# Kernel optimization log

Measured on AMD Instinct MI355X. Metric: run time of the kernel, lower is better.

Reference implementation:

```python
import jax, jax.numpy as jnp
import numpy as np

B, C, H, W = 128, 8, 144, 144
TW, OG = 5, 2          # token_window, off_grid
NCLS, DT = 6, 256      # num_cls, dim_token
ITC = C * H * TW       # in_token_channel = 5760
EPS = 1e-5


def setup_inputs() -> dict:
    key = jax.random.key(0)
    ks = jax.random.split(key, 40)
    n = jax.random.normal
    u = jax.random.uniform
    CW = C * W  # 1152
    inp = {
        'x': n(ks[0], (B, C, H, W), jnp.float32),
        # ext head: Conv1d(1152,256,1) -> BN(256) -> Conv1d(256,2,1)
        'ext_w1': n(ks[1], (256, CW)) * 0.02, 'ext_b1': jnp.zeros((256,)),
        'ext_g': jnp.ones((256,)), 'ext_bb': jnp.zeros((256,)),
        'ext_m': n(ks[2], (256,)) * 0.1, 'ext_v': u(ks[3], (256,), minval=0.5, maxval=1.5),
        'ext_w2': n(ks[4], (2, 256)) * 0.05, 'ext_b2': jnp.zeros((2,)),
        # cls head: Conv1d(1152,256,1) -> BN(256) -> Conv1d(256,144,1)
        'cls_w1': n(ks[5], (256, CW)) * 0.02, 'cls_b1': jnp.zeros((256,)),
        'cls_g': jnp.ones((256,)), 'cls_bb': jnp.zeros((256,)),
        'cls_m': n(ks[6], (256,)) * 0.1, 'cls_v': u(ks[7], (256,), minval=0.5, maxval=1.5),
        'cls_w2': n(ks[8], (W, 256)) * 0.05, 'cls_b2': jnp.zeros((W,)),
        # to_token Linear(5760,256) and class embeddings
        'tok_w': n(ks[9], (ITC, DT)) * 0.01, 'tok_b': jnp.zeros((DT,)),
        'emb': n(ks[10], (NCLS, DT)),
        # transformer (depth=1, heads=2, dim_head=32 -> inner=64)
        'ln1_g': jnp.ones((DT,)), 'ln1_b': jnp.zeros((DT,)),
        'qkv_w': n(ks[11], (DT, 3 * 64)) * 0.05,
        'out_w': n(ks[12], (64, DT)) * 0.05, 'out_b': jnp.zeros((DT,)),
        'ln2_g': jnp.ones((DT,)), 'ln2_b': jnp.zeros((DT,)),
        'ff_w1': n(ks[13], (DT, 512)) * 0.05, 'ff_b1': jnp.zeros((512,)),
        'ff_w2': n(ks[14], (512, DT)) * 0.05, 'ff_b2': jnp.zeros((DT,)),
        'lnf_g': jnp.ones((DT,)), 'lnf_b': jnp.zeros((DT,)),
        'fin_w': n(ks[15], (DT, ITC)) * 0.02, 'fin_b': jnp.zeros((ITC,)),
    }
    return inp


def _ln(z, g, b):
    mu = jnp.mean(z, -1, keepdims=True)
    var = jnp.var(z, -1, keepdims=True)
    return (z - mu) * jax.lax.rsqrt(var + EPS) * g + b


def reference(x, ext_w1, ext_b1, ext_g, ext_bb, ext_m, ext_v, ext_w2, ext_b2,
              cls_w1, cls_b1, cls_g, cls_bb, cls_m, cls_v, cls_w2, cls_b2,
              tok_w, tok_b, emb,
              ln1_g, ln1_b, qkv_w, out_w, out_b,
              ln2_g, ln2_b, ff_w1, ff_b1, ff_w2, ff_b2,
              lnf_g, lnf_b, fin_w, fin_b):

    def head(row, w1, b1, g, bet, m, v, w2, b2):
        # row: [B, C*W, H]; 1x1 conv = per-position GEMM, BN in eval mode
        h = jnp.einsum('oc,bch->boh', w1, row) + b1[:, None]
        h = (h - m[:, None]) * jax.lax.rsqrt(v[:, None] + EPS) * g[:, None] + bet[:, None]
        h = jnp.einsum('oc,bch->boh', w2, h) + b2[:, None]
        return jnp.transpose(h, (0, 2, 1))  # [B, H, out]

    def heads_on(xx):
        # 'b c h w -> b (c w) h' (c major, w minor)
        row = jnp.transpose(xx, (0, 1, 3, 2)).reshape(B, C * W, H)
        e = jax.nn.softmax(head(row, ext_w1, ext_b1, ext_g, ext_bb, ext_m, ext_v, ext_w2, ext_b2), axis=2)
        c = jax.nn.softmax(head(row, cls_w1, cls_b1, cls_g, cls_bb, cls_m, cls_v, cls_w2, cls_b2), axis=2)
        return e, c

    ext, cls = heads_on(x)
    xp = jnp.pad(x, ((0, 0), (0, 0), (0, 0), (OG, OG)))  # [B,C,H,W+4]

    argmax_col = jnp.argmax(cls, axis=2)                  # [B,H]
    idx = argmax_col[:, :, None] + jnp.arange(TW)         # window in padded coords

    def transformer(t):  # t: [B, N, DT]
        z = _ln(t, ln1_g, ln1_b)
        q, k, v = jnp.split(z @ qkv_w, 3, axis=-1)
        sp = lambda a: a.reshape(B, -1, 2, 32).transpose(0, 2, 1, 3)  # b h n d
        q, k, v = sp(q), sp(k), sp(v)
        att = jax.nn.softmax(jnp.einsum('bhnd,bhmd->bhnm', q, k) * (32 ** -0.5), axis=-1)
        o = jnp.einsum('bhnm,bhmd->bhnd', att, v).transpose(0, 2, 1, 3).reshape(B, -1, 64)
        t = o @ out_w + out_b + t
        z = _ln(t, ln2_g, ln2_b)
        t = jax.nn.gelu(z @ ff_w1 + ff_b1, approximate=False) @ ff_w2 + ff_b2 + t
        t = _ln(t, lnf_g, lnf_b)
        return (t @ fin_w + fin_b).reshape(B, -1, C, H, TW)  # [B,N,C,H,TW]

    def refine(xpad):
        g_idx = jnp.broadcast_to(idx[:, None], (B, C, H, TW))
        patches = jnp.take_along_axis(xpad, g_idx, axis=3)    # [B,C,H,TW]
        tok = patches.reshape(B, -1) @ tok_w + tok_b          # [B,DT]
        tokens = tok[:, None, :] + emb[None]                  # [B,NCLS,DT]
        refined = transformer(tokens)                         # [B,NCLS,C,H,TW]
        xpt = jnp.transpose(xpad, (0, 2, 3, 1))               # [B,H,Wp,C]
        bb = jnp.arange(B)[:, None, None]
        hh = jnp.arange(H)[None, :, None]
        for i in range(NCLS):
            xpt = xpt.at[bb, hh, idx].set(jnp.transpose(refined[:, i], (0, 2, 3, 1)))
        return jnp.transpose(xpt, (0, 3, 1, 2))

    xp = jax.lax.cond(jnp.mean(ext[:, :, 0]) > 0.3, refine, lambda a: a, xp)
    x2 = xp[:, :, :, OG:W + OG]
    ext2, cls2 = heads_on(x2)
    return ext, cls, ext2, cls2
```

## Files before the change

kernel.cpp:

```cpp
#include <hip/hip_runtime.h>
#include <math.h>

#define EPSF 1e-5f
#define GAPTH 2e-4f
#define NKS 2
#define KSL 576
#define RROWS 18432
#define LPAD 44


typedef __attribute__((ext_vector_type(8))) short short8v;
typedef __attribute__((ext_vector_type(4))) float f32x4;
typedef unsigned short ushort;
typedef unsigned int uint;

__device__ inline ushort f2bf(float f) {
    uint u = __float_as_uint(f);
    uint r = (u + 0x7FFFu + ((u >> 16) & 1u)) >> 16;
    return (ushort)r;
}
__device__ inline float bf2f(ushort h) { return __uint_as_float(((uint)h) << 16); }

__global__ __launch_bounds__(256) void wcomb_build(
    const float* __restrict__ w1e, const float* __restrict__ b1e, const float* __restrict__ ge,
    const float* __restrict__ bbe, const float* __restrict__ me, const float* __restrict__ ve,
    const float* __restrict__ w2e, const float* __restrict__ b2e,
    const float* __restrict__ w1c, const float* __restrict__ b1c, const float* __restrict__ gc,
    const float* __restrict__ bbc, const float* __restrict__ mc, const float* __restrict__ vc,
    const float* __restrict__ w2c, const float* __restrict__ b2c,
    float* __restrict__ Wc32, ushort* __restrict__ Wchi, ushort* __restrict__ Wclo,
    float* __restrict__ cconst, int* __restrict__ cand_count)
{
    __shared__ float coef[256];
    __shared__ float csum[4];
    const int j = blockIdx.x, kq = blockIdx.y, tid = threadIdx.x;
    const int lane = tid & 63, wid = tid >> 6;

    if (j == 0 && kq == 0 && tid == 0) *cand_count = 0;

    const float *w1 = nullptr, *w2row = nullptr, *b1 = nullptr, *g = nullptr,
                *bb = nullptr, *m = nullptr, *v = nullptr;
    float b2v = 0.f;
    int valid = 0;
    if (j < 144) {
        valid = 1; w1 = w1c; w2row = w2c + (size_t)j * 256;
        b1 = b1c; g = gc; bb = bbc; m = mc; v = vc; b2v = b2c[j];
    } else if (j < 146) {
        valid = 1; w1 = w1e; w2row = w2e + (size_t)(j - 144) * 256;
        b1 = b1e; g = ge; bb = bbe; m = me; v = ve; b2v = b2e[j - 144];
    }

    float cf = 0.f, cc = 0.f;
    if (valid) {
        float s = g[tid] * rsqrtf(v[tid] + EPSF);
        float w2v = w2row[tid];
        cf = w2v * s;
        cc = w2v * ((b1[tid] - m[tid]) * s + bb[tid]);
    }
    coef[tid] = cf;
    if (kq == 0) {
        float t = cc;
#pragma unroll
        for (int off = 32; off; off >>= 1) t += __shfl_xor(t, off);
        if (lane == 0) csum[wid] = t;
    }
    __syncthreads();
    if (kq == 0 && tid == 0)
        cconst[j] = valid ? ((csum[0] + csum[1]) + (csum[2] + csum[3]) + b2v) : 0.f;

    for (int k = kq * 288 + tid; k < (kq + 1) * 288; k += 256) {
        float acc = 0.f;
        if (valid) {
            float a0 = 0.f, a1 = 0.f, a2 = 0.f, a3 = 0.f;
            for (int o = 0; o < 256; o += 4) {
                a0 += coef[o]     * w1[(size_t)o * 1152 + k];
                a1 += coef[o + 1] * w1[(size_t)(o + 1) * 1152 + k];
                a2 += coef[o + 2] * w1[(size_t)(o + 2) * 1152 + k];
                a3 += coef[o + 3] * w1[(size_t)(o + 3) * 1152 + k];
            }
            acc = (a0 + a1) + (a2 + a3);
        }
        Wc32[(size_t)j * 1152 + k] = acc;
        ushort hi = f2bf(acc);
        Wchi[(size_t)j * 1152 + k] = hi;
        Wclo[(size_t)j * 1152 + k] = f2bf(acc - bf2f(hi));
    }
}

__global__ __launch_bounds__(256) void transpose3(
    const float* __restrict__ s0, float* __restrict__ d0,
    const float* __restrict__ s1, float* __restrict__ d1,
    const float* __restrict__ s2, float* __restrict__ d2)
{
    const float* src; float* dst; int R, Cc;
    if (blockIdx.z == 0)      { src = s0; dst = d0; R = 256; Cc = 1152; }
    else if (blockIdx.z == 1) { src = s1; dst = d1; R = 144; Cc = 256;
                                if (blockIdx.x >= 8 || blockIdx.y >= 5) return; }
    else                      { src = s2; dst = d2; R = 160; Cc = 1152;
                                if (blockIdx.y >= 5) return; }
    __shared__ float tile[32][33];
    const int rb = blockIdx.y * 32, cb = blockIdx.x * 32;
    const int tx = threadIdx.x & 31, ty = threadIdx.x >> 5;
#pragma unroll
    for (int i = ty; i < 32; i += 8) {
        int r = rb + i, c = cb + tx;
        tile[i][tx] = (r < R && c < Cc) ? src[(size_t)r * Cc + c] : 0.f;
    }
    __syncthreads();
#pragma unroll
    for (int i = ty; i < 32; i += 8) {
        int c = cb + i, r = rb + tx;
        if (c < Cc && r < R) dst[(size_t)c * R + r] = tile[tx][i];
    }
}

__global__ __launch_bounds__(256) void logits_gemm(
    const float* __restrict__ x, const ushort* __restrict__ Wchi, const ushort* __restrict__ Wclo,
    float* __restrict__ logits_part)
{
    __shared__ ushort Ahi[64][LPAD], Alo[64][LPAD], Bhi[160][LPAD], Blo[160][LPAD];
    const int tid = threadIdx.x;
    const int lane = tid & 63, wid = tid >> 6;
    const int wm = wid & 1, wn = wid >> 1;
    const int rb = blockIdx.x * 64;
    const int ks = blockIdx.y;
    const int kbase = ks * KSL;
    const int NIT = KSL / 32;

    const int rl = tid >> 2, kk = (tid & 3) << 3;
    const int arow = rb + rl;
    const int ab = arow / 144, ahh = arow - ab * 144;

    const int br0 = tid >> 2, bk0 = (tid & 3) << 3;
    const int br2 = 128 + (tid >> 2), bk2 = (tid & 3) << 3;

    float av[8];
    short8v vbh0, vbl0, vbh1, vbl1, vbh2, vbl2;

    auto LOAD = [&](int kb) {
        int k1 = kb + kk, c1 = k1 / 144, w1 = k1 - c1 * 144;
        const float4 t0 = *reinterpret_cast<const float4*>(
            x + (((size_t)(ab * 8 + c1) * 144 + ahh) * 144 + w1));
        const float4 t1 = *reinterpret_cast<const float4*>(
            x + (((size_t)(ab * 8 + c1) * 144 + ahh) * 144 + w1 + 4));
        av[0] = t0.x; av[1] = t0.y; av[2] = t0.z; av[3] = t0.w;
        av[4] = t1.x; av[5] = t1.y; av[6] = t1.z; av[7] = t1.w;
        size_t o0 = (size_t)br0 * 1152 + kb + bk0;
        vbh0 = *reinterpret_cast<const short8v*>(Wchi + o0);
        vbl0 = *reinterpret_cast<const short8v*>(Wclo + o0);
        size_t o1 = (size_t)(br0 + 64) * 1152 + kb + bk0;
        vbh1 = *reinterpret_cast<const short8v*>(Wchi + o1);
        vbl1 = *reinterpret_cast<const short8v*>(Wclo + o1);
        if (tid < 128) {
            size_t o2 = (size_t)br2 * 1152 + kb + bk2;
            vbh2 = *reinterpret_cast<const short8v*>(Wchi + o2);
            vbl2 = *reinterpret_cast<const short8v*>(Wclo + o2);
        }
    };

    auto STORE = [&]() {
        short8v hv, lv;
#pragma unroll
        for (int q = 0; q < 8; q++) {
            ushort h = f2bf(av[q]);
            hv[q] = (short)h;
            lv[q] = (short)f2bf(av[q] - bf2f(h));
        }
        *reinterpret_cast<short8v*>(&Ahi[rl][kk]) = hv;
        *reinterpret_cast<short8v*>(&Alo[rl][kk]) = lv;
        *reinterpret_cast<short8v*>(&Bhi[br0][bk0]) = vbh0;
        *reinterpret_cast<short8v*>(&Blo[br0][bk0]) = vbl0;
        *reinterpret_cast<short8v*>(&Bhi[br0 + 64][bk0]) = vbh1;
        *reinterpret_cast<short8v*>(&Blo[br0 + 64][bk0]) = vbl1;
        if (tid < 128) {
            *reinterpret_cast<short8v*>(&Bhi[br2][bk2]) = vbh2;
            *reinterpret_cast<short8v*>(&Blo[br2][bk2]) = vbl2;
        }
    };

    f32x4 acc[2][5];
#pragma unroll
    for (int mt = 0; mt < 2; mt++)
#pragma unroll
        for (int nt = 0; nt < 5; nt++) acc[mt][nt] = (f32x4){0.f, 0.f, 0.f, 0.f};

    const int fr = lane & 15, fg = (lane >> 4) << 3;

    LOAD(kbase);
    for (int t = 0; t < NIT; t++) {
        STORE();
        __syncthreads();
        if (t < NIT - 1) LOAD(kbase + (t + 1) * 32);
        short8v ah0 = *reinterpret_cast<const short8v*>(&Ahi[wm * 32 + fr][fg]);
        short8v al0 = *reinterpret_cast<const short8v*>(&Alo[wm * 32 + fr][fg]);
        short8v ah1 = *reinterpret_cast<const short8v*>(&Ahi[wm * 32 + 16 + fr][fg]);
        short8v al1 = *reinterpret_cast<const short8v*>(&Alo[wm * 32 + 16 + fr][fg]);
#pragma unroll
        for (int nt = 0; nt < 5; nt++) {
            short8v bh = *reinterpret_cast<const short8v*>(&Bhi[wn * 80 + nt * 16 + fr][fg]);
            short8v bl = *reinterpret_cast<const short8v*>(&Blo[wn * 80 + nt * 16 + fr][fg]);
            acc[0][nt] = __builtin_amdgcn_mfma_f32_16x16x32_bf16(ah0, bh, acc[0][nt], 0, 0, 0);
            acc[0][nt] = __builtin_amdgcn_mfma_f32_16x16x32_bf16(ah0, bl, acc[0][nt], 0, 0, 0);
            acc[0][nt] = __builtin_amdgcn_mfma_f32_16x16x32_bf16(al0, bh, acc[0][nt], 0, 0, 0);
            acc[1][nt] = __builtin_amdgcn_mfma_f32_16x16x32_bf16(ah1, bh, acc[1][nt], 0, 0, 0);
            acc[1][nt] = __builtin_amdgcn_mfma_f32_16x16x32_bf16(ah1, bl, acc[1][nt], 0, 0, 0);
            acc[1][nt] = __builtin_amdgcn_mfma_f32_16x16x32_bf16(al1, bh, acc[1][nt], 0, 0, 0);
        }
        __syncthreads();
    }

    float* base = logits_part + (size_t)ks * RROWS * 160;
#pragma unroll
    for (int mt = 0; mt < 2; mt++) {
#pragma unroll
        for (int nt = 0; nt < 5; nt++) {
            int gcol = wn * 80 + nt * 16 + fr;
            if (gcol < 146) {
                float* dst = base + (size_t)(rb + wm * 32 + mt * 16 + ((lane >> 4) << 2)) * 160 + gcol;
#pragma unroll
                for (int i = 0; i < 4; i++)
                    dst[(size_t)i * 160] = acc[mt][nt][i];
            }
        }
    }
}

template<int DELTA>
__global__ __launch_bounds__(256) void softmax_heads(
    const float* __restrict__ logits_part, const float* __restrict__ cconst,
    float* __restrict__ out_cls, float* __restrict__ out_ext,
    int* __restrict__ amax, float* __restrict__ partials,
    int* __restrict__ cand_count, int* __restrict__ cand_list,
    const float* __restrict__ x, const float* __restrict__ WcT,
    const float* __restrict__ refined5, const int* __restrict__ flag)
{
    __shared__ float ps[4];
    __shared__ float dL[4][148];
    __shared__ float dsh[4][40];
    __shared__ int   ksh[4][40];
    const int r4 = threadIdx.x >> 6, lane = threadIdx.x & 63;
    const int row = blockIdx.x * 4 + r4;

    if (DELTA) {
        const int fl = *flag;
        if (fl) {
            const int b = row / 144, hh = row - b * 144;
            const int a = amax[row];
            if (lane < 40) {
                int c = lane / 5, tw = lane - c * 5;
                int w = a - 2 + tw;
                float d = 0.f; int k = 0;
                if (w >= 0 && w < 144) {
                    k = c * 144 + w;
                    d = refined5[(size_t)b * 5760 + (c * 144 + hh) * 5 + tw]
                      - x[((size_t)(b * 8 + c) * 144 + hh) * 144 + w];
                }
                dsh[r4][lane] = d; ksh[r4][lane] = k;
            }
            __syncthreads();
#pragma unroll
            for (int rj = 0; rj < 3; rj++) {
                int j = lane + rj * 64;
                if (j < 146) {
                    float acc = 0.f;
#pragma unroll 8
                    for (int i = 0; i < 40; i++)
                        acc += WcT[(size_t)ksh[r4][i] * 160 + j] * dsh[r4][i];
                    dL[r4][j] = acc;
                }
            }
        } else {
#pragma unroll
            for (int rj = 0; rj < 3; rj++) {
                int j = lane + rj * 64;
                if (j < 146) dL[r4][j] = 0.f;
            }
        }
        __syncthreads();
    }

    const float* L0 = logits_part + (size_t)row * 160;
    const float* L1 = L0 + (size_t)RROWS * 160;
    float v0 = L0[lane] + L1[lane] + cconst[lane];
    float v1 = L0[lane + 64] + L1[lane + 64] + cconst[lane + 64];
    float v2 = (lane < 16) ? (L0[lane + 128] + L1[lane + 128] + cconst[lane + 128])
                           : -3.0e38f;
    if (DELTA) {
        v0 += dL[r4][lane];
        v1 += dL[r4][lane + 64];
        if (lane < 16) v2 += dL[r4][lane + 128];
    }
    float m = v0; int mi = lane;
    if (v1 > m) { m = v1; mi = lane + 64; }
    if (v2 > m) { m = v2; mi = lane + 128; }
    float m1 = v0, m2 = -3.0e38f;
    if (v1 > m1) { m2 = m1; m1 = v1; } else m2 = v1;
    if (v2 > m1) { m2 = m1; m1 = v2; } else m2 = fmaxf(m2, v2);
#pragma unroll
    for (int off = 32; off; off >>= 1) {
        float om = __shfl_xor(m, off);
        int   oi = __shfl_xor(mi, off);
        if (om > m || (om == m && oi < mi)) { m = om; mi = oi; }
        float om1 = __shfl_xor(m1, off);
        float om2 = __shfl_xor(m2, off);
        float nm1 = fmaxf(m1, om1);
        m2 = fmaxf(fminf(m1, om1), fmaxf(m2, om2));
        m1 = nm1;
    }
    float e0 = expf(v0 - m), e1 = expf(v1 - m);
    float e2 = (lane < 16) ? expf(v2 - m) : 0.f;
    float s = e0 + e1 + e2;
#pragma unroll
    for (int off = 32; off; off >>= 1) s += __shfl_xor(s, off);
    float inv = 1.f / s;
    float* O = out_cls + (size_t)row * 144;
    O[lane] = e0 * inv;
    O[lane + 64] = e1 * inv;
    if (lane < 16) O[lane + 128] = e2 * inv;

    float l0 = L0[144] + L1[144] + cconst[144];
    float l1 = L0[145] + L1[145] + cconst[145];
    if (DELTA) { l0 += dL[r4][144]; l1 += dL[r4][145]; }
    float mx = fmaxf(l0, l1);
    float ee0 = expf(l0 - mx), ee1 = expf(l1 - mx);
    float einv = 1.f / (ee0 + ee1);
    float p0 = ee0 * einv;
    if (lane == 0) {
        out_ext[(size_t)row * 2] = p0;
        out_ext[(size_t)row * 2 + 1] = ee1 * einv;
        if (amax != nullptr && !DELTA) {
            amax[row] = mi;
            if (m1 - m2 < GAPTH) {
                int slot = atomicAdd(cand_count, 1);
                cand_list[slot] = row;
            }
        }
    }
    if (partials != nullptr) {
        if (lane == 0) ps[r4] = p0;
        __syncthreads();
        if (threadIdx.x == 0) partials[blockIdx.x] = (ps[0] + ps[1]) + (ps[2] + ps[3]);
    }
}

__global__ __launch_bounds__(256) void reduce_flag(const float* __restrict__ partials, int n,
                                                   int* __restrict__ flag)
{
    __shared__ float sm[256];
    int tid = threadIdx.x;
    float s = 0.f;
    for (int i = tid; i < n; i += 256) s += partials[i];
    sm[tid] = s; __syncthreads();
    for (int off = 128; off; off >>= 1) {
        if (tid < off) sm[tid] += sm[tid + off];
        __syncthreads();
    }
    if (tid == 0) *flag = (sm[0] * (1.f / 18432.f) > 0.3f) ? 1 : 0;
}

__global__ __launch_bounds__(256) void fixup_list(
    const int* __restrict__ cand_count, const int* __restrict__ cand_list,
    const float* __restrict__ x,
    const float* __restrict__ w1cT, const float* __restrict__ b1c,
    const float* __restrict__ gc, const float* __restrict__ bbc,
    const float* __restrict__ mc, const float* __restrict__ vc,
    const float* __restrict__ w2cT, const float* __restrict__ b2c,
    int* __restrict__ amax)
{
    __shared__ float xrow[1152];
    __shared__ float hsh[256];
    __shared__ float Lsh[144];
    const int tid = threadIdx.x;
    const int n = *cand_count;

    for (int ci = blockIdx.x; ci < n; ci += gridDim.x) {
        const int row = cand_list[ci];
        const int b = row / 144, hh = row - b * 144;
        for (int e = tid; e < 1152; e += 256) {
            int c = e / 144, w = e - c * 144;
            xrow[e] = x[(((size_t)(b * 8 + c) * 144 + hh) * 144) + w];
        }
        __syncthreads();
        {
            float a0 = 0.f, a1 = 0.f, a2 = 0.f, a3 = 0.f;
#pragma unroll 4
            for (int k = 0; k < 1152; k += 4) {
                a0 += w1cT[(size_t)k * 256 + tid] * xrow[k];
                a1 += w1cT[(size_t)(k + 1) * 256 + tid] * xrow[k + 1];
                a2 += w1cT[(size_t)(k + 2) * 256 + tid] * xrow[k + 2];
                a3 += w1cT[(size_t)(k + 3) * 256 + tid] * xrow[k + 3];
            }
            float a = (a0 + a1) + (a2 + a3);
            float sc = gc[tid] * rsqrtf(vc[tid] + EPSF);
            hsh[tid] = (a + b1c[tid] - mc[tid]) * sc + bbc[tid];
        }
        __syncthreads();
        if (tid < 144) {
            float a0 = 0.f, a1 = 0.f, a2 = 0.f, a3 = 0.f;
#pragma unroll 4
            for (int k = 0; k < 256; k += 4) {
                a0 += w2cT[(size_t)k * 144 + tid] * hsh[k];
                a1 += w2cT[(size_t)(k + 1) * 144 + tid] * hsh[k + 1];
                a2 += w2cT[(size_t)(k + 2) * 144 + tid] * hsh[k + 2];
                a3 += w2cT[(size_t)(k + 3) * 144 + tid] * hsh[k + 3];
            }
            Lsh[tid] = (a0 + a1) + (a2 + a3) + b2c[tid];
        }
        __syncthreads();
        if (tid == 0) {
            int bi = 0; float bv = Lsh[0];
            for (int j = 1; j < 144; j++) if (Lsh[j] > bv) { bv = Lsh[j]; bi = j; }
            amax[row] = bi;
        }
        __syncthreads();
    }
}

__global__ __launch_bounds__(256) void tok_partial(const float* __restrict__ x,
    const int* __restrict__ amax, const float* __restrict__ tok_w, float* __restrict__ tpart)
{
    __shared__ float P[720];
    __shared__ int ash[144];
    int b = blockIdx.x, c = blockIdx.y, tid = threadIdx.x;
    if (tid < 144) ash[tid] = amax[b * 144 + tid];
    __syncthreads();
    for (int e = tid; e < 720; e += 256) {
        int hh = e / 5, tw = e - hh * 5;
        int w = ash[hh] + tw - 2;
        P[e] = (w >= 0 && w < 144) ? x[(((size_t)(b * 8 + c) * 144 + hh) * 144) + w] : 0.f;
    }
    __syncthreads();
    const float* wbase = tok_w + (size_t)c * 720 * 256;
    float a0 = 0.f, a1 = 0.f, a2 = 0.f, a3 = 0.f;
    for (int k = 0; k < 720; k += 4) {
        a0 += P[k]     * wbase[(size_t)k * 256 + tid];
        a1 += P[k + 1] * wbase[(size_t)(k + 1) * 256 + tid];
        a2 += P[k + 2] * wbase[(size_t)(k + 2) * 256 + tid];
        a3 += P[k + 3] * wbase[(size_t)(k + 3) * 256 + tid];
    }
    tpart[((size_t)b * 8 + c) * 256 + tid] = (a0 + a1) + (a2 + a3);
}

__global__ __launch_bounds__(256) void qkv_gemm(
    const float* __restrict__ tpart, const float* __restrict__ tok_b,
    const float* __restrict__ emb,
    const float* __restrict__ ln1_g, const float* __restrict__ ln1_b,
    const float* __restrict__ qkv_w,
    float* __restrict__ qkbuf, float* __restrict__ sbuf)
{
    __shared__ float zrow[256];
    __shared__ float r8[8];
    const int b = blockIdx.x, y = blockIdx.y, tid = threadIdx.x;
    const int i = (y < 6) ? y : 5;
    const int lane = tid & 63, wv = tid >> 6;
    const int g4 = tid >> 2, l4 = tid & 3;

    float a = tok_b[tid];
#pragma unroll
    for (int ks = 0; ks < 8; ks++) a += tpart[((size_t)b * 8 + ks) * 256 + tid];
    if (y == 6) sbuf[(size_t)b * 256 + tid] = a;

    float v = a + emb[i * 256 + tid];
    float s1 = v, s2 = v * v;
#pragma unroll
    for (int off = 32; off; off >>= 1) { s1 += __shfl_down(s1, off); s2 += __shfl_down(s2, off); }
    if (lane == 0) { r8[wv * 2] = s1; r8[wv * 2 + 1] = s2; }
    __syncthreads();
    float t1 = (r8[0] + r8[2]) + (r8[4] + r8[6]);
    float t2 = (r8[1] + r8[3]) + (r8[5] + r8[7]);
    float mu = t1 * (1.f / 256.f);
    float var = t2 * (1.f / 256.f) - mu * mu;
    zrow[tid] = (v - mu) * rsqrtf(var + EPSF) * ln1_g[tid] + ln1_b[tid];
    __syncthreads();

    if (y < 6) {
        for (int tt = g4; tt < 128; tt += 64) {
            const int c = 64 + tt;
            float acc = 0.f;
#pragma unroll 8
            for (int j = 0; j < 64; j++) {
                int k = l4 + 4 * j;
                acc += zrow[k] * qkv_w[(size_t)k * 192 + c];
            }
            acc += __shfl_xor(acc, 1);
            acc += __shfl_xor(acc, 2);
            if (l4 == 0) qkbuf[((size_t)b * 6 + i) * 192 + c] = acc;
        }
    } else {
        const int c = g4;
        float acc = 0.f;
#pragma unroll 8
        for (int j = 0; j < 64; j++) {
            int k = l4 + 4 * j;
            acc += zrow[k] * qkv_w[(size_t)k * 192 + c];
        }
        acc += __shfl_xor(acc, 1);
        acc += __shfl_xor(acc, 2);
        if (l4 == 0) qkbuf[((size_t)b * 6 + 5) * 192 + c] = acc;
    }
}

__global__ __launch_bounds__(256) void attn_out(
    const float* __restrict__ qkbuf, const float* __restrict__ sbuf,
    const float* __restrict__ emb,
    const float* __restrict__ out_w, const float* __restrict__ out_b,
    const float* __restrict__ ln2_g, const float* __restrict__ ln2_b,
    float* __restrict__ z2_5, float* __restrict__ t5buf)
{
    __shared__ float qk[6][192];
    __shared__ float att[2][6];
    __shared__ float o5[64];
    __shared__ float t5[256];
    __shared__ float stat[2];
    const int b = blockIdx.x, tid = threadIdx.x;
    const int lane = tid & 63, wv = tid >> 6;
    const int g4 = tid >> 2, l4 = tid & 3;

    for (int e = tid; e < 1152; e += 256)
        qk[e / 192][e - (e / 192) * 192] = qkbuf[(size_t)b * 1152 + e];
    __syncthreads();

    if (tid < 12) {
        int h = tid / 6, j = tid - h * 6;
        float a = 0.f;
#pragma unroll
        for (int d = 0; d < 32; d++) a += qk[5][h * 32 + d] * qk[j][64 + h * 32 + d];
        att[h][j] = a * 0.17677669529663687f;
    }
    __syncthreads();
    if (tid < 2) {
        float m = -3.0e38f;
        for (int j = 0; j < 6; j++) m = fmaxf(m, att[tid][j]);
        float ssum = 0.f;
        for (int j = 0; j < 6; j++) { float e = expf(att[tid][j] - m); att[tid][j] = e; ssum += e; }
        float inv = 1.f / ssum;
        for (int j = 0; j < 6; j++) att[tid][j] *= inv;
    }
    __syncthreads();
    if (tid < 64) {
        int h = tid >> 5;
        float a = 0.f;
#pragma unroll
        for (int j = 0; j < 6; j++) a += att[h][j] * qk[j][128 + tid];
        o5[tid] = a;
    }
    __syncthreads();

    for (int tt = g4; tt < 256; tt += 64) {
        float a = 0.f;
#pragma unroll
        for (int j = 0; j < 16; j++) {
            int d = l4 + 4 * j;
            a += o5[d] * out_w[(size_t)d * 256 + tt];
        }
        a += __shfl_xor(a, 1);
        a += __shfl_xor(a, 2);
        if (l4 == 0)
            t5[tt] = a + out_b[tt] + sbuf[(size_t)b * 256 + tt] + emb[5 * 256 + tt];
    }
    __syncthreads();

    if (wv == 0) {
        float s1 = 0.f, s2 = 0.f;
#pragma unroll
        for (int q = 0; q < 4; q++) { float vv = t5[lane + 64 * q]; s1 += vv; s2 += vv * vv; }
#pragma unroll
        for (int off = 32; off; off >>= 1) { s1 += __shfl_xor(s1, off); s2 += __shfl_xor(s2, off); }
        if (lane == 0) {
            float mu = s1 * (1.f / 256.f);
            float var = s2 * (1.f / 256.f) - mu * mu;
            stat[0] = mu; stat[1] = rsqrtf(var + EPSF);
        }
    }
    __syncthreads();
    t5buf[(size_t)b * 256 + tid] = t5[tid];
    z2_5[(size_t)b * 256 + tid] = (t5[tid] - stat[0]) * stat[1] * ln2_g[tid] + ln2_b[tid];
}

__global__ __launch_bounds__(256) void ff1_gelu(
    const float* __restrict__ z2_5, const float* __restrict__ ff_w1,
    const float* __restrict__ ff_b1, float* __restrict__ f5)
{
    __shared__ float zsh[256];
    const int b = blockIdx.x, q = blockIdx.y, tid = threadIdx.x;
    const int g4 = tid >> 2, l4 = tid & 3;
    zsh[tid] = z2_5[(size_t)b * 256 + tid];
    __syncthreads();
    for (int tt = g4; tt < 128; tt += 64) {
        const int jj = q * 128 + tt;
        float a = 0.f;
#pragma unroll 8
        for (int j = 0; j < 64; j++) {
            int k = l4 + 4 * j;
            a += zsh[k] * ff_w1[(size_t)k * 512 + jj];
        }
        a += __shfl_xor(a, 1);
        a += __shfl_xor(a, 2);
        if (l4 == 0) {
            a += ff_b1[jj];
            f5[(size_t)b * 512 + jj] = 0.5f * a * (1.f + erff(a * 0.70710678118654752f));
        }
    }
}

__global__ __launch_bounds__(256) void ff2_half(
    const float* __restrict__ f5, const float* __restrict__ ff_w2,
    const float* __restrict__ ff_b2, const float* __restrict__ t5buf,
    float* __restrict__ t6)
{
    __shared__ float fsh[512];
    const int b = blockIdx.x, h = blockIdx.y, tid = threadIdx.x;
    const int g4 = tid >> 2, l4 = tid & 3;
    fsh[tid] = f5[(size_t)b * 512 + tid];
    fsh[tid + 256] = f5[(size_t)b * 512 + tid + 256];
    __syncthreads();
    for (int tt = g4; tt < 128; tt += 64) {
        const int o = h * 128 + tt;
        float a = 0.f;
#pragma unroll 8
        for (int j = 0; j < 128; j++) {
            int k = l4 + 4 * j;
            a += fsh[k] * ff_w2[(size_t)k * 256 + o];
        }
        a += __shfl_xor(a, 1);
        a += __shfl_xor(a, 2);
        if (l4 == 0)
            t6[(size_t)b * 256 + o] = a + ff_b2[o] + t5buf[(size_t)b * 256 + o];
    }
}

__global__ __launch_bounds__(256) void fin_gemm(const float* __restrict__ t6,
    const float* __restrict__ lnf_g, const float* __restrict__ lnf_b,
    const float* __restrict__ fin_w, const float* __restrict__ fin_b,
    float* __restrict__ refined5)
{
    __shared__ float tf[16][256];
    __shared__ float stat[16][2];
    int tid = threadIdx.x;
    int nb = blockIdx.x * 256 + tid;
    int bg = blockIdx.y * 16;
    for (int e = tid; e < 4096; e += 256)
        tf[e >> 8][e & 255] = t6[(size_t)(bg + (e >> 8)) * 256 + (e & 255)];
    __syncthreads();
    {
        int r = tid >> 4, sl = tid & 15;
        float s1 = 0.f, s2 = 0.f;
#pragma unroll
        for (int j = 0; j < 16; j++) {
            float vv = tf[r][sl + 16 * j];
            s1 += vv; s2 += vv * vv;
        }
#pragma unroll
        for (int off = 8; off; off >>= 1) { s1 += __shfl_xor(s1, off); s2 += __shfl_xor(s2, off); }
        if (sl == 0) {
            float mu = s1 * (1.f / 256.f);
            float var = s2 * (1.f / 256.f) - mu * mu;
            stat[r][0] = mu; stat[r][1] = rsqrtf(var + EPSF);
        }
    }
    __syncthreads();
    for (int e = tid; e < 4096; e += 256) {
        int r = e >> 8, c = e & 255;
        tf[r][c] = (tf[r][c] - stat[r][0]) * stat[r][1] * lnf_g[c] + lnf_b[c];
    }
    __syncthreads();
    if (nb < 5760) {
        float acc[16];
#pragma unroll
        for (int bb = 0; bb < 16; bb++) acc[bb] = 0.f;
        for (int k = 0; k < 256; k++) {
            float wv = fin_w[(size_t)k * 5760 + nb];
#pragma unroll
            for (int bb = 0; bb < 16; bb++) acc[bb] += tf[bb][k] * wv;
        }
        float fb = fin_b[nb];
#pragma unroll
        for (int bb = 0; bb < 16; bb++)
            refined5[(size_t)(bg + bb) * 5760 + nb] = acc[bb] + fb;
    }
}

extern "C" void kernel_launch(void* const* d_in, const int* in_sizes, int n_in,
                              void* d_out, int out_size, void* d_ws, size_t ws_size,
                              hipStream_t stream)
{
    const float* x      = (const float*)d_in[0];
    const float* ext_w1 = (const float*)d_in[1];
    const float* ext_b1 = (const float*)d_in[2];
    const float* ext_g  = (const float*)d_in[3];
    const float* ext_bb = (const float*)d_in[4];
    const float* ext_m  = (const float*)d_in[5];
    const float* ext_v  = (const float*)d_in[6];
    const float* ext_w2 = (const float*)d_in[7];
    const float* ext_b2 = (const float*)d_in[8];
    const float* cls_w1 = (const float*)d_in[9];
    const float* cls_b1 = (const float*)d_in[10];
    const float* cls_g  = (const float*)d_in[11];
    const float* cls_bb = (const float*)d_in[12];
    const float* cls_m  = (const float*)d_in[13];
    const float* cls_v  = (const float*)d_in[14];
    const float* cls_w2 = (const float*)d_in[15];
    const float* cls_b2 = (const float*)d_in[16];
    const float* tok_w  = (const float*)d_in[17];
    const float* tok_b  = (const float*)d_in[18];
    const float* emb    = (const float*)d_in[19];
    const float* ln1_g  = (const float*)d_in[20];
    const float* ln1_b  = (const float*)d_in[21];
    const float* qkv_w  = (const float*)d_in[22];
    const float* out_w  = (const float*)d_in[23];
    const float* out_b  = (const float*)d_in[24];
    const float* ln2_g  = (const float*)d_in[25];
    const float* ln2_b  = (const float*)d_in[26];
    const float* ff_w1  = (const float*)d_in[27];
    const float* ff_b1  = (const float*)d_in[28];
    const float* ff_w2  = (const float*)d_in[29];
    const float* ff_b2  = (const float*)d_in[30];
    const float* lnf_g  = (const float*)d_in[31];
    const float* lnf_b  = (const float*)d_in[32];
    const float* fin_w  = (const float*)d_in[33];
    const float* fin_b  = (const float*)d_in[34];

    float* out = (float*)d_out;
    float* ws  = (float*)d_ws;

    float*  Wc32     = ws;
    float*  cconst   = ws + 184320;
    ushort* Wchi     = (ushort*)(ws + 184480);
    ushort* Wclo     = (ushort*)(ws + 276640);
    float*  logitsP  = ws + 368800;
    float*  partials = ws + 6267040;
    float*  refined5 = ws + 6435488;
    float*  tpart    = ws + 7172768;
    int*    amax     = (int*)(ws + 7434912);
    int*    flag     = (int*)(ws + 7453344);
    int*    cand_cnt = (int*)(ws + 7453345);
    int*    cand_lst = (int*)(ws + 7453346);
    float*  w1cT     = ws + 7471780;
    float*  w2cT     = ws + 7766692;
    float*  WcT      = ws + 7803556;
    float*  sbuf     = ws + 8184484;
    float*  qkbuf    = ws + 8217252;
    float*  z2_5     = ws + 8364708;
    float*  t5buf    = ws + 8397476;
    float*  f5buf    = ws + 8430244;
    float*  t6buf    = ws + 8495780;

    float* out_ext  = out;
    float* out_cls  = out + 36864;
    float* out_ext2 = out + 2691072;
    float* out_cls2 = out + 2727936;

    dim3 blk(256);

    wcomb_build<<<dim3(160, 4), blk, 0, stream>>>(
        ext_w1, ext_b1, ext_g, ext_bb, ext_m, ext_v, ext_w2, ext_b2,
        cls_w1, cls_b1, cls_g, cls_bb, cls_m, cls_v, cls_w2, cls_b2,
        Wc32, Wchi, Wclo, cconst, cand_cnt);
    transpose3<<<dim3(36, 8, 3), blk, 0, stream>>>(cls_w1, w1cT, cls_w2, w2cT, Wc32, WcT);

    logits_gemm<<<dim3(288, NKS), blk, 0, stream>>>(x, Wchi, Wclo, logitsP);
    softmax_heads<0><<<4608, blk, 0, stream>>>(logitsP, cconst, out_cls, out_ext, amax, partials,
        cand_cnt, cand_lst, nullptr, nullptr, nullptr, nullptr);
    reduce_flag<<<1, blk, 0, stream>>>(partials, 4608, flag);
    fixup_list<<<256, blk, 0, stream>>>(cand_cnt, cand_lst, x,
        w1cT, cls_b1, cls_g, cls_bb, cls_m, cls_v, w2cT, cls_b2, amax);

    tok_partial<<<dim3(128, 8), blk, 0, stream>>>(x, amax, tok_w, tpart);
    qkv_gemm<<<dim3(128, 7), blk, 0, stream>>>(tpart, tok_b, emb, ln1_g, ln1_b, qkv_w,
        qkbuf, sbuf);
    attn_out<<<128, blk, 0, stream>>>(qkbuf, sbuf, emb, out_w, out_b, ln2_g, ln2_b, z2_5, t5buf);
    ff1_gelu<<<dim3(128, 4), blk, 0, stream>>>(z2_5, ff_w1, ff_b1, f5buf);
    ff2_half<<<dim3(128, 2), blk, 0, stream>>>(f5buf, ff_w2, ff_b2, t5buf, t6buf);
    fin_gemm<<<dim3(23, 8), blk, 0, stream>>>(t6buf, lnf_g, lnf_b, fin_w, fin_b, refined5);

    softmax_heads<1><<<4608, blk, 0, stream>>>(logitsP, cconst, out_cls2, out_ext2, amax, nullptr,
        nullptr, nullptr, x, WcT, refined5, flag);
}
```

Measured before the change: 262.2 us.

## Fuse first softmax heads into logits GEMM and drop split-K

Removes the two-way split-K of the logits GEMM so each block computes the full K=1152 reduction, then stages the 64x160 logit tile in LDS (aliased over the GEMM buffers) and runs the first softmax, argmax, candidate detection and partial-sum reduction in the same kernel. The second softmax pass now reads the single bias-added logits buffer instead of summing two partials plus the constant. This eliminates one launch and the round trip of split-K partials, but halves the GEMM grid to 288 blocks, which lowers parallelism and lengthens each block's K loop.

```diff
diff --git a/kernel.cpp b/kernel.cpp
--- a/kernel.cpp
+++ b/kernel.cpp
@@ -3,10 +3,9 @@
 
 #define EPSF 1e-5f
 #define GAPTH 2e-4f
-#define NKS 2
-#define KSL 576
 #define RROWS 18432
 #define LPAD 44
+#define SPAD 165
 
 
 typedef __attribute__((ext_vector_type(8))) short short8v;
@@ -114,18 +113,25 @@
     }
 }
 
-__global__ __launch_bounds__(256) void logits_gemm(
+__global__ __launch_bounds__(256) void logits_gemm_sm(
     const float* __restrict__ x, const ushort* __restrict__ Wchi, const ushort* __restrict__ Wclo,
-    float* __restrict__ logits_part)
-{
-    __shared__ ushort Ahi[64][LPAD], Alo[64][LPAD], Bhi[160][LPAD], Blo[160][LPAD];
+    const float* __restrict__ cconst,
+    float* __restrict__ logits, float* __restrict__ out_cls, float* __restrict__ out_ext,
+    int* __restrict__ amax, float* __restrict__ partials,
+    int* __restrict__ cand_count, int* __restrict__ cand_list)
+{
+    union LdsU {
+        struct { ushort Ahi[64][LPAD], Alo[64][LPAD], Bhi[160][LPAD], Blo[160][LPAD]; } g;
+        float S[64][SPAD];
+    };
+    __shared__ LdsU u;
+    __shared__ float ps4[4];
+
     const int tid = threadIdx.x;
     const int lane = tid & 63, wid = tid >> 6;
     const int wm = wid & 1, wn = wid >> 1;
     const int rb = blockIdx.x * 64;
-    const int ks = blockIdx.y;
-    const int kbase = ks * KSL;
-    const int NIT = KSL / 32;
+    const int NIT = 1152 / 32;
 
     const int rl = tid >> 2, kk = (tid & 3) << 3;
     const int arow = rb + rl;
@@ -166,15 +172,15 @@
             hv[q] = (short)h;
             lv[q] = (short)f2bf(av[q] - bf2f(h));
         }
-        *reinterpret_cast<short8v*>(&Ahi[rl][kk]) = hv;
-        *reinterpret_cast<short8v*>(&Alo[rl][kk]) = lv;
-        *reinterpret_cast<short8v*>(&Bhi[br0][bk0]) = vbh0;
-        *reinterpret_cast<short8v*>(&Blo[br0][bk0]) = vbl0;
-        *reinterpret_cast<short8v*>(&Bhi[br0 + 64][bk0]) = vbh1;
-        *reinterpret_cast<short8v*>(&Blo[br0 + 64][bk0]) = vbl1;
+        *reinterpret_cast<short8v*>(&u.g.Ahi[rl][kk]) = hv;
+        *reinterpret_cast<short8v*>(&u.g.Alo[rl][kk]) = lv;
+        *reinterpret_cast<short8v*>(&u.g.Bhi[br0][bk0]) = vbh0;
+        *reinterpret_cast<short8v*>(&u.g.Blo[br0][bk0]) = vbl0;
+        *reinterpret_cast<short8v*>(&u.g.Bhi[br0 + 64][bk0]) = vbh1;
+        *reinterpret_cast<short8v*>(&u.g.Blo[br0 + 64][bk0]) = vbl1;
         if (tid < 128) {
-            *reinterpret_cast<short8v*>(&Bhi[br2][bk2]) = vbh2;
-            *reinterpret_cast<short8v*>(&Blo[br2][bk2]) = vbl2;
+            *reinterpret_cast<short8v*>(&u.g.Bhi[br2][bk2]) = vbh2;
+            *reinterpret_cast<short8v*>(&u.g.Blo[br2][bk2]) = vbl2;
         }
     };
 
@@ -186,19 +192,19 @@
 
     const int fr = lane & 15, fg = (lane >> 4) << 3;
 
-    LOAD(kbase);
+    LOAD(0);
     for (int t = 0; t < NIT; t++) {
         STORE();
         __syncthreads();
-        if (t < NIT - 1) LOAD(kbase + (t + 1) * 32);
-        short8v ah0 = *reinterpret_cast<const short8v*>(&Ahi[wm * 32 + fr][fg]);
-        short8v al0 = *reinterpret_cast<const short8v*>(&Alo[wm * 32 + fr][fg]);
-        short8v ah1 = *reinterpret_cast<const short8v*>(&Ahi[wm * 32 + 16 + fr][fg]);
-        short8v al1 = *reinterpret_cast<const short8v*>(&Alo[wm * 32 + 16 + fr][fg]);
+        if (t < NIT - 1) LOAD((t + 1) * 32);
+        short8v ah0 = *reinterpret_cast<const short8v*>(&u.g.Ahi[wm * 32 + fr][fg]);
+        short8v al0 = *reinterpret_cast<const short8v*>(&u.g.Alo[wm * 32 + fr][fg]);
+        short8v ah1 = *reinterpret_cast<const short8v*>(&u.g.Ahi[wm * 32 + 16 + fr][fg]);
+        short8v al1 = *reinterpret_cast<const short8v*>(&u.g.Alo[wm * 32 + 16 + fr][fg]);
 #pragma unroll
         for (int nt = 0; nt < 5; nt++) {
-            short8v bh = *reinterpret_cast<const short8v*>(&Bhi[wn * 80 + nt * 16 + fr][fg]);
-            short8v bl = *reinterpret_cast<const short8v*>(&Blo[wn * 80 + nt * 16 + fr][fg]);
+            short8v bh = *reinterpret_cast<const short8v*>(&u.g.Bhi[wn * 80 + nt * 16 + fr][fg]);
+            short8v bl = *reinterpret_cast<const short8v*>(&u.g.Blo[wn * 80 + nt * 16 + fr][fg]);
             acc[0][nt] = __builtin_amdgcn_mfma_f32_16x16x32_bf16(ah0, bh, acc[0][nt], 0, 0, 0);
             acc[0][nt] = __builtin_amdgcn_mfma_f32_16x16x32_bf16(ah0, bl, acc[0][nt], 0, 0, 0);
             acc[0][nt] = __builtin_amdgcn_mfma_f32_16x16x32_bf16(al0, bh, acc[0][nt], 0, 0, 0);
@@ -209,103 +215,140 @@
         __syncthreads();
     }
 
-    float* base = logits_part + (size_t)ks * RROWS * 160;
 #pragma unroll
     for (int mt = 0; mt < 2; mt++) {
 #pragma unroll
         for (int nt = 0; nt < 5; nt++) {
             int gcol = wn * 80 + nt * 16 + fr;
-            if (gcol < 146) {
-                float* dst = base + (size_t)(rb + wm * 32 + mt * 16 + ((lane >> 4) << 2)) * 160 + gcol;
-#pragma unroll
-                for (int i = 0; i < 4; i++)
-                    dst[(size_t)i * 160] = acc[mt][nt][i];
+            float cc = (gcol < 146) ? cconst[gcol] : 0.f;
+            int rbase = wm * 32 + mt * 16 + ((lane >> 4) << 2);
+#pragma unroll
+            for (int i = 0; i < 4; i++) {
+                float val = acc[mt][nt][i] + cc;
+                u.S[rbase + i][gcol] = val;
+                if (gcol < 146)
+                    logits[(size_t)(rb + rbase + i) * 160 + gcol] = val;
             }
         }
     }
-}
-
-template<int DELTA>
-__global__ __launch_bounds__(256) void softmax_heads(
-    const float* __restrict__ logits_part, const float* __restrict__ cconst,
+    __syncthreads();
+
+    float psum = 0.f;
+    for (int rr = 0; rr < 16; rr++) {
+        const int r = wid * 16 + rr;
+        float v0 = u.S[r][lane];
+        float v1 = u.S[r][lane + 64];
+        float v2 = (lane < 16) ? u.S[r][128 + lane] : -3.0e38f;
+        float m = v0; int mi = lane;
+        if (v1 > m) { m = v1; mi = lane + 64; }
+        if (v2 > m) { m = v2; mi = lane + 128; }
+        float m1 = v0, m2 = -3.0e38f;
+        if (v1 > m1) { m2 = m1; m1 = v1; } else m2 = v1;
+        if (v2 > m1) { m2 = m1; m1 = v2; } else m2 = fmaxf(m2, v2);
+#pragma unroll
+        for (int off = 32; off; off >>= 1) {
+            float om = __shfl_xor(m, off);
+            int   oi = __shfl_xor(mi, off);
+            if (om > m || (om == m && oi < mi)) { m = om; mi = oi; }
+            float om1 = __shfl_xor(m1, off);
+            float om2 = __shfl_xor(m2, off);
+            float nm1 = fmaxf(m1, om1);
+            m2 = fmaxf(fminf(m1, om1), fmaxf(m2, om2));
+            m1 = nm1;
+        }
+        float e0 = expf(v0 - m), e1 = expf(v1 - m);
+        float e2 = (lane < 16) ? expf(v2 - m) : 0.f;
+        float s = e0 + e1 + e2;
+#pragma unroll
+        for (int off = 32; off; off >>= 1) s += __shfl_xor(s, off);
+        float inv = 1.f / s;
+        float* O = out_cls + (size_t)(rb + r) * 144;
+        O[lane] = e0 * inv;
+        O[lane + 64] = e1 * inv;
+        if (lane < 16) O[128 + lane] = e2 * inv;
+
+        float l0 = u.S[r][144], l1 = u.S[r][145];
+        float mx = fmaxf(l0, l1);
+        float ee0 = expf(l0 - mx), ee1 = expf(l1 - mx);
+        float einv = 1.f / (ee0 + ee1);
+        float p0 = ee0 * einv;
+        if (lane == 0) {
+            out_ext[(size_t)(rb + r) * 2] = p0;
+            out_ext[(size_t)(rb + r) * 2 + 1] = ee1 * einv;
+            amax[rb + r] = mi;
+            if (m1 - m2 < GAPTH) {
+                int slot = atomicAdd(cand_count, 1);
+                cand_list[slot] = rb + r;
+            }
+            psum += p0;
+        }
+    }
+    if (lane == 0) ps4[wid] = psum;
+    __syncthreads();
+    if (tid == 0) partials[blockIdx.x] = (ps4[0] + ps4[1]) + (ps4[2] + ps4[3]);
+}
+
+__global__ __launch_bounds__(256) void softmax_delta(
+    const float* __restrict__ logits,
     float* __restrict__ out_cls, float* __restrict__ out_ext,
-    int* __restrict__ amax, float* __restrict__ partials,
-    int* __restrict__ cand_count, int* __restrict__ cand_list,
+    const int* __restrict__ amax,
     const float* __restrict__ x, const float* __restrict__ WcT,
     const float* __restrict__ refined5, const int* __restrict__ flag)
 {
-    __shared__ float ps[4];
     __shared__ float dL[4][148];
     __shared__ float dsh[4][40];
     __shared__ int   ksh[4][40];
     const int r4 = threadIdx.x >> 6, lane = threadIdx.x & 63;
     const int row = blockIdx.x * 4 + r4;
 
-    if (DELTA) {
-        const int fl = *flag;
-        if (fl) {
-            const int b = row / 144, hh = row - b * 144;
-            const int a = amax[row];
-            if (lane < 40) {
-                int c = lane / 5, tw = lane - c * 5;
-                int w = a - 2 + tw;
-                float d = 0.f; int k = 0;
-                if (w >= 0 && w < 144) {
-                    k = c * 144 + w;
-                    d = refined5[(size_t)b * 5760 + (c * 144 + hh) * 5 + tw]
-                      - x[((size_t)(b * 8 + c) * 144 + hh) * 144 + w];
-                }
-                dsh[r4][lane] = d; ksh[r4][lane] = k;
+    const int fl = *flag;
+    if (fl) {
+        const int b = row / 144, hh = row - b * 144;
+        const int a = amax[row];
+        if (lane < 40) {
+            int c = lane / 5, tw = lane - c * 5;
+            int w = a - 2 + tw;
+            float d = 0.f; int k = 0;
+            if (w >= 0 && w < 144) {
+                k = c * 144 + w;
+                d = refined5[(size_t)b * 5760 + (c * 144 + hh) * 5 + tw]
+                  - x[((size_t)(b * 8 + c) * 144 + hh) * 144 + w];
             }
-            __syncthreads();
-#pragma unroll
-            for (int rj = 0; rj < 3; rj++) {
-                int j = lane + rj * 64;
-                if (j < 146) {
-                    float acc = 0.f;
+            dsh[r4][lane] = d; ksh[r4][lane] = k;
+        }
+        __syncthreads();
+#pragma unroll
+        for (int rj = 0; rj < 3; rj++) {
+            int j = lane + rj * 64;
+            if (j < 146) {
+                float acc = 0.f;
 #pragma unroll 8
-                    for (int i = 0; i < 40; i++)
-                        acc += WcT[(size_t)ksh[r4][i] * 160 + j] * dsh[r4][i];
-                    dL[r4][j] = acc;
-                }
+                for (int i = 0; i < 40; i++)
+                    acc += WcT[(size_t)ksh[r4][i] * 160 + j] * dsh[r4][i];
+                dL[r4][j] = acc;
             }
-        } else {
-#pragma unroll
-            for (int rj = 0; rj < 3; rj++) {
-                int j = lane + rj * 64;
-                if (j < 146) dL[r4][j] = 0.f;
-            }
-        }
-        __syncthreads();
-    }
-
-    const float* L0 = logits_part + (size_t)row * 160;
-    const float* L1 = L0 + (size_t)RROWS * 160;
-    float v0 = L0[lane] + L1[lane] + cconst[lane];
-    float v1 = L0[lane + 64] + L1[lane + 64] + cconst[lane + 64];
-    float v2 = (lane < 16) ? (L0[lane + 128] + L1[lane + 128] + cconst[lane + 128])
-                           : -3.0e38f;
-    if (DELTA) {
-        v0 += dL[r4][lane];
-        v1 += dL[r4][lane + 64];
-        if (lane < 16) v2 += dL[r4][lane + 128];
-    }
+        }
+    } else {
+#pragma unroll
+        for (int rj = 0; rj < 3; rj++) {
+            int j = lane + rj * 64;
+            if (j < 146) dL[r4][j] = 0.f;
+        }
+    }
+    __syncthreads();
+
+    const float* L0 = logits + (size_t)row * 160;
+    float v0 = L0[lane] + dL[r4][lane];
+    float v1 = L0[lane + 64] + dL[r4][lane + 64];
+    float v2 = (lane < 16) ? (L0[lane + 128] + dL[r4][lane + 128]) : -3.0e38f;
     float m = v0; int mi = lane;
     if (v1 > m) { m = v1; mi = lane + 64; }
     if (v2 > m) { m = v2; mi = lane + 128; }
-    float m1 = v0, m2 = -3.0e38f;
-    if (v1 > m1) { m2 = m1; m1 = v1; } else m2 = v1;
-    if (v2 > m1) { m2 = m1; m1 = v2; } else m2 = fmaxf(m2, v2);
 #pragma unroll
     for (int off = 32; off; off >>= 1) {
         float om = __shfl_xor(m, off);
         int   oi = __shfl_xor(mi, off);
         if (om > m || (om == m && oi < mi)) { m = om; mi = oi; }
-        float om1 = __shfl_xor(m1, off);
-        float om2 = __shfl_xor(m2, off);
-        float nm1 = fmaxf(m1, om1);
-        m2 = fmaxf(fminf(m1, om1), fmaxf(m2, om2));
-        m1 = nm1;
     }
     float e0 = expf(v0 - m), e1 = expf(v1 - m);
     float e2 = (lane < 16) ? expf(v2 - m) : 0.f;
@@ -318,28 +361,14 @@
     O[lane + 64] = e1 * inv;
     if (lane < 16) O[lane + 128] = e2 * inv;
 
-    float l0 = L0[144] + L1[144] + cconst[144];
-    float l1 = L0[145] + L1[145] + cconst[145];
-    if (DELTA) { l0 += dL[r4][144]; l1 += dL[r4][145]; }
+    float l0 = L0[144] + dL[r4][144];
+    float l1 = L0[145] + dL[r4][145];
     float mx = fmaxf(l0, l1);
     float ee0 = expf(l0 - mx), ee1 = expf(l1 - mx);
     float einv = 1.f / (ee0 + ee1);
-    float p0 = ee0 * einv;
     if (lane == 0) {
-        out_ext[(size_t)row * 2] = p0;
+        out_ext[(size_t)row * 2] = ee0 * einv;
         out_ext[(size_t)row * 2 + 1] = ee1 * einv;
-        if (amax != nullptr && !DELTA) {
-            amax[row] = mi;
-            if (m1 - m2 < GAPTH) {
-                int slot = atomicAdd(cand_count, 1);
-                cand_list[slot] = row;
-            }
-        }
-    }
-    if (partials != nullptr) {
-        if (lane == 0) ps[r4] = p0;
-        __syncthreads();
-        if (threadIdx.x == 0) partials[blockIdx.x] = (ps[0] + ps[1]) + (ps[2] + ps[3]);
     }
 }
 
@@ -727,7 +756,7 @@
     float*  cconst   = ws + 184320;
     ushort* Wchi     = (ushort*)(ws + 184480);
     ushort* Wclo     = (ushort*)(ws + 276640);
-    float*  logitsP  = ws + 368800;
+    float*  logits   = ws + 368800;
     float*  partials = ws + 6267040;
     float*  refined5 = ws + 6435488;
     float*  tpart    = ws + 7172768;
@@ -758,10 +787,9 @@
         Wc32, Wchi, Wclo, cconst, cand_cnt);
     transpose3<<<dim3(36, 8, 3), blk, 0, stream>>>(cls_w1, w1cT, cls_w2, w2cT, Wc32, WcT);
 
-    logits_gemm<<<dim3(288, NKS), blk, 0, stream>>>(x, Wchi, Wclo, logitsP);
-    softmax_heads<0><<<4608, blk, 0, stream>>>(logitsP, cconst, out_cls, out_ext, amax, partials,
-        cand_cnt, cand_lst, nullptr, nullptr, nullptr, nullptr);
-    reduce_flag<<<1, blk, 0, stream>>>(partials, 4608, flag);
+    logits_gemm_sm<<<288, blk, 0, stream>>>(x, Wchi, Wclo, cconst,
+        logits, out_cls, out_ext, amax, partials, cand_cnt, cand_lst);
+    reduce_flag<<<1, blk, 0, stream>>>(partials, 288, flag);
     fixup_list<<<256, blk, 0, stream>>>(cand_cnt, cand_lst, x,
         w1cT, cls_b1, cls_g, cls_bb, cls_m, cls_v, w2cT, cls_b2, amax);
 
@@ -773,6 +801,6 @@
     ff2_half<<<dim3(128, 2), blk, 0, stream>>>(f5buf, ff_w2, ff_b2, t5buf, t6buf);
     fin_gemm<<<dim3(23, 8), blk, 0, stream>>>(t6buf, lnf_g, lnf_b, fin_w, fin_b, refined5);
 
-    softmax_heads<1><<<4608, blk, 0, stream>>>(logitsP, cconst, out_cls2, out_ext2, amax, nullptr,
-        nullptr, nullptr, x, WcT, refined5, flag);
-}
+    softmax_delta<<<4608, blk, 0, stream>>>(logits, out_cls2, out_ext2, amax,
+        x, WcT, refined5, flag);
+}
```

Measured after the change: 297.0 us. +13.3%, slower.
